# Kernel optimization log

Measured on AMD Instinct MI355X. Metric: run time of the kernel, lower is better.

The kernel has to match this reference:

```python
import jax, jax.numpy as jnp
import numpy as np

B, V = 256, 128000
NEG_INF = jnp.float32(-1e30)


def setup_inputs() -> dict:
    key = jax.random.key(0)
    k1, k2, k3 = jax.random.split(key, 3)
    logits = jax.random.normal(k1, (B, V), dtype=jnp.float32) * 2.0
    k = jax.random.randint(k2, (B,), 1, 65)                     # top-k in [1, 64]
    p = 0.5 + 0.5 * jax.random.uniform(k3, (B,), jnp.float32)   # top-p in [0.5, 1.0]
    return {"logits": logits, "k": k, "p": p}


def reference(logits, k, p):
    # softmax over vocab (rbln_top_k_top_p_sample: probs = softmax(logits))
    probs = jax.nn.softmax(logits, axis=-1)                      # [B, V]

    # sort probs descending (torch.ops.rbln.top_k_top_p semantics)
    order = jnp.argsort(-probs, axis=-1)                         # [B, V]
    sp = jnp.take_along_axis(probs, order, axis=-1)              # sorted probs, desc

    ranks = jnp.arange(V)
    topk_mask = ranks[None, :] < k[:, None]                      # keep top-k ranks

    csum = jnp.cumsum(sp, axis=-1)
    # keep tokens whose cumulative mass BEFORE them is < p (always keeps rank 0)
    topp_mask = (csum - sp) < p[:, None]

    keep = topk_mask & topp_mask                                 # [B, V] in sorted space
    filtered = jnp.where(keep, sp, 0.0)
    filtered = filtered / jnp.sum(filtered, axis=-1, keepdims=True)

    # sample from the renormalized filtered distribution (seed=42 as in module)
    logp = jnp.where(keep, jnp.log(jnp.maximum(filtered, 1e-38)), NEG_INF)
    sampled_rank = jax.random.categorical(jax.random.key(42), logp, axis=-1)  # [B]
    sampled = jnp.take_along_axis(order, sampled_rank[:, None], axis=-1)[:, 0]
    return sampled
```

## Files before the change

kernel.cpp:

```cpp
#include <hip/hip_runtime.h>
#include <stdint.h>

#define V 128000
#define V4 (V / 4)
#define BROWS 256
#define CAP 2048
#define NTHREADS 1024
#define T0 16.0f

__device__ __forceinline__ unsigned rotl32(unsigned x, int d) {
  return (x << d) | (x >> (32 - d));
}

__device__ __forceinline__ uint2 threefry2x32(unsigned x0, unsigned x1) {
  const unsigned k0 = 0u, k1 = 42u;
  const unsigned k2 = k0 ^ k1 ^ 0x1BD11BDAu;
  x0 += k0; x1 += k1;
#define TF_RND(r) { x0 += x1; x1 = rotl32(x1, r); x1 ^= x0; }
  TF_RND(13) TF_RND(15) TF_RND(26) TF_RND(6)
  x0 += k1; x1 += k2 + 1u;
  TF_RND(17) TF_RND(29) TF_RND(16) TF_RND(24)
  x0 += k2; x1 += k0 + 2u;
  TF_RND(13) TF_RND(15) TF_RND(26) TF_RND(6)
  x0 += k0; x1 += k1 + 3u;
  TF_RND(17) TF_RND(29) TF_RND(16) TF_RND(24)
  x0 += k1; x1 += k2 + 4u;
  TF_RND(13) TF_RND(15) TF_RND(26) TF_RND(6)
  x0 += k2; x1 += k0 + 5u;
#undef TF_RND
  return make_uint2(x0, x1);
}

__device__ __forceinline__ float gumbel_at(unsigned flat) {
  uint2 r = threefry2x32(0u, flat);
  unsigned bits = r.x ^ r.y;
  float f = __uint_as_float((bits >> 9) | 0x3F800000u) - 1.0f;
  const float TINY = 1.17549435e-38f;
  float u = fmaxf(TINY, f + TINY);
  return -logf(-logf(u));
}

__device__ __forceinline__ unsigned fkey(float v) {
  unsigned u = __float_as_uint(v);
  return (u & 0x80000000u) ? ~u : (u | 0x80000000u);
}
__device__ __forceinline__ float fkey_inv(unsigned u) {
  unsigned r = (u & 0x80000000u) ? (u & 0x7FFFFFFFu) : ~u;
  return __uint_as_float(r);
}

extern "C" __global__ void __launch_bounds__(NTHREADS)
topk_topp_sample_kernel(const float* __restrict__ logits,
                        const int* __restrict__ kin,
                        const float* __restrict__ pin,
                        int* __restrict__ out) {
  const int b = blockIdx.x;
  const int tid = threadIdx.x;

  __shared__ unsigned long long cand[CAP];
  __shared__ unsigned long long topkeys[64];
  __shared__ float zpart[NTHREADS / 64];
  __shared__ float sh_sp[64];
  __shared__ float sh_g[64];
  __shared__ int sh_idx[64];
  __shared__ int cnt;
  __shared__ float shZ;

  const float4* row4 = (const float4*)(logits + (size_t)b * V);
  float T = 6.0f;

  if (tid == 0) cnt = 0;
  __syncthreads();

  const float L2E = 1.44269504088896340736f;
  const float NB  = -16.0f * 1.44269504088896340736f;
  float zs0 = 0.0f, zs1 = 0.0f;

#define PROCV(vv, ii)                                                          \
  {                                                                            \
    float4 v = (vv);                                                           \
    zs0 += __builtin_amdgcn_exp2f(__builtin_fmaf(v.x, L2E, NB));               \
    zs1 += __builtin_amdgcn_exp2f(__builtin_fmaf(v.y, L2E, NB));               \
    zs0 += __builtin_amdgcn_exp2f(__builtin_fmaf(v.z, L2E, NB));               \
    zs1 += __builtin_amdgcn_exp2f(__builtin_fmaf(v.w, L2E, NB));               \
    int base = (ii) * 4;                                                       \
    if (v.x > T) { int pos = atomicAdd(&cnt, 1); if (pos < CAP) cand[pos] = ((unsigned long long)fkey(v.x) << 32) | (unsigned long long)(unsigned)(~(unsigned)(base + 0)); } \
    if (v.y > T) { int pos = atomicAdd(&cnt, 1); if (pos < CAP) cand[pos] = ((unsigned long long)fkey(v.y) << 32) | (unsigned long long)(unsigned)(~(unsigned)(base + 1)); } \
    if (v.z > T) { int pos = atomicAdd(&cnt, 1); if (pos < CAP) cand[pos] = ((unsigned long long)fkey(v.z) << 32) | (unsigned long long)(unsigned)(~(unsigned)(base + 2)); } \
    if (v.w > T) { int pos = atomicAdd(&cnt, 1); if (pos < CAP) cand[pos] = ((unsigned long long)fkey(v.w) << 32) | (unsigned long long)(unsigned)(~(unsigned)(base + 3)); } \
  }

  {
    int i = tid;
    for (; i + NTHREADS < V4; i += 2 * NTHREADS) {
      float4 a = row4[i];
      float4 c = row4[i + NTHREADS];
      PROCV(a, i);
      PROCV(c, i + NTHREADS);
    }
    if (i < V4) {
      float4 a = row4[i];
      PROCV(a, i);
    }
  }
  float s = zs0 + zs1;

#pragma unroll
  for (int off = 32; off > 0; off >>= 1) s += __shfl_down(s, off);
  if ((tid & 63) == 0) zpart[tid >> 6] = s;
  __syncthreads();
  if (tid == 0) {
    float z = 0.0f;
    for (int w = 0; w < NTHREADS / 64; ++w) z += zpart[w];
    shZ = z;
  }
  __syncthreads();

  int attempts = 0;
  while (true) {
    int n = cnt;
    if ((n >= 64 && n <= CAP) || attempts >= 24) break;
    T = (n < 64) ? (T - 2.0f) : (T + 1.0f);
    ++attempts;
    __syncthreads();
    if (tid == 0) cnt = 0;
    __syncthreads();
    for (int i = tid; i < V4; i += NTHREADS) {
      float4 v = row4[i];
      int base = i * 4;
      if (v.x > T) { int pos = atomicAdd(&cnt, 1); if (pos < CAP) cand[pos] = ((unsigned long long)fkey(v.x) << 32) | (unsigned long long)(unsigned)(~(unsigned)(base + 0)); }
      if (v.y > T) { int pos = atomicAdd(&cnt, 1); if (pos < CAP) cand[pos] = ((unsigned long long)fkey(v.y) << 32) | (unsigned long long)(unsigned)(~(unsigned)(base + 1)); }
      if (v.z > T) { int pos = atomicAdd(&cnt, 1); if (pos < CAP) cand[pos] = ((unsigned long long)fkey(v.z) << 32) | (unsigned long long)(unsigned)(~(unsigned)(base + 2)); }
      if (v.w > T) { int pos = atomicAdd(&cnt, 1); if (pos < CAP) cand[pos] = ((unsigned long long)fkey(v.w) << 32) | (unsigned long long)(unsigned)(~(unsigned)(base + 3)); }
    }
    __syncthreads();
  }

  int N = cnt < CAP ? cnt : CAP;

  for (int i = tid; i < N; i += NTHREADS) {
    unsigned long long ki = cand[i];
    int rank = 0;
    for (int j = 0; j < N; ++j) rank += (cand[j] > ki) ? 1 : 0;
    if (rank < 64) topkeys[rank] = ki;
  }
  __syncthreads();

  int M = N < 64 ? N : 64;

  if (tid < M) {
    unsigned long long key = topkeys[tid];
    float v = fkey_inv((unsigned)(key >> 32));
    sh_sp[tid] = expf(v - T0) / shZ;
    sh_idx[tid] = (int)(~((unsigned)(key & 0xFFFFFFFFull)));
    sh_g[tid] = gumbel_at((unsigned)((size_t)b * V + tid));
  }
  __syncthreads();

  if (tid == 0) {
    int kk = kin[b];
    float pp = pin[b];
    float c = 0.0f, S = 0.0f;
    unsigned long long keepmask = 0ull;
    for (int r = 0; r < M; ++r) {
      float sp = sh_sp[r];
      c += sp;
      if (r < kk && (c - sp) < pp) {
        S += sp;
        keepmask |= (1ull << r);
      }
    }
    float best = -1e38f;
    int besti = sh_idx[0];
    for (int r = 0; r < M; ++r) {
      if (!(keepmask & (1ull << r))) continue;
      float lp = logf(fmaxf(sh_sp[r] / S, 1e-38f));
      float y = lp + sh_g[r];
      if (y > best) { best = y; besti = sh_idx[r]; }
    }
    out[b] = besti;
  }
}

extern "C" void kernel_launch(void* const* d_in, const int* in_sizes, int n_in,
                              void* d_out, int out_size, void* d_ws, size_t ws_size,
                              hipStream_t stream) {
  const float* logits = (const float*)d_in[0];
  const int* k = (const int*)d_in[1];
  const float* p = (const float*)d_in[2];
  int* out = (int*)d_out;
  (void)in_sizes; (void)n_in; (void)out_size; (void)d_ws; (void)ws_size;
  topk_topp_sample_kernel<<<BROWS, NTHREADS, 0, stream>>>(logits, k, p, out);
}
```

Baseline: 202.7 us.

## Split row scan across eight segment blocks, then merge candidates per row

The single 1024-thread-block-per-row kernel becomes two kernels. The first launches eight 256-thread blocks per row, and each computes a partial softmax denominator and gathers logits above a threshold into a workspace. The second kernel merges those partial results per row, rank-sorts the candidates and samples, falling back to a full-row rescan if any segment overflows or too few candidates were found. The aim is more blocks in flight to saturate memory bandwidth, at the cost of a second launch and a workspace round-trip.

Measured after the change: 213.8 us. 5.5% more time.

```diff
diff --git a/kernel.cpp b/kernel.cpp
--- a/kernel.cpp
+++ b/kernel.cpp
@@ -2,11 +2,17 @@
 #include <stdint.h>
 
 #define V 128000
-#define V4 (V / 4)
 #define BROWS 256
-#define CAP 2048
-#define NTHREADS 1024
+#define SEGS 8
+#define SEGLEN (V / SEGS)
+#define SEG4 (SEGLEN / 4)
+#define CAPSEG 512
+#define CAPB 4096
+#define NT_A 256
+#define NT_B 256
 #define T0 16.0f
+
+typedef unsigned long long u64;
 
 __device__ __forceinline__ unsigned rotl32(unsigned x, int d) {
   return (x << d) | (x >> (32 - d));
@@ -49,29 +55,24 @@
   return __uint_as_float(r);
 }
 
-extern "C" __global__ void __launch_bounds__(NTHREADS)
-topk_topp_sample_kernel(const float* __restrict__ logits,
-                        const int* __restrict__ kin,
-                        const float* __restrict__ pin,
-                        int* __restrict__ out) {
-  const int b = blockIdx.x;
+extern "C" __global__ void __launch_bounds__(NT_A)
+scan_seg_kernel(const float* __restrict__ logits,
+                int* __restrict__ g_cnt, float* __restrict__ g_z,
+                u64* __restrict__ g_cand) {
+  const int bid = blockIdx.x;
+  const int row = bid >> 3, seg = bid & 7;
   const int tid = threadIdx.x;
 
-  __shared__ unsigned long long cand[CAP];
-  __shared__ unsigned long long topkeys[64];
-  __shared__ float zpart[NTHREADS / 64];
-  __shared__ float sh_sp[64];
-  __shared__ float sh_g[64];
-  __shared__ int sh_idx[64];
-  __shared__ int cnt;
-  __shared__ float shZ;
-
-  const float4* row4 = (const float4*)(logits + (size_t)b * V);
-  float T = 6.0f;
-
-  if (tid == 0) cnt = 0;
-  __syncthreads();
-
+  __shared__ u64 lcand[CAPSEG];
+  __shared__ int lcnt;
+  __shared__ float wz[NT_A / 64];
+
+  if (tid == 0) lcnt = 0;
+  __syncthreads();
+
+  const float4* p4 = (const float4*)(logits + (size_t)row * V) + seg * SEG4;
+  const int ebase = seg * SEGLEN;
+  const float T = 6.0f;
   const float L2E = 1.44269504088896340736f;
   const float NB  = -16.0f * 1.44269504088896340736f;
   float zs0 = 0.0f, zs1 = 0.0f;
@@ -83,63 +84,120 @@
     zs1 += __builtin_amdgcn_exp2f(__builtin_fmaf(v.y, L2E, NB));               \
     zs0 += __builtin_amdgcn_exp2f(__builtin_fmaf(v.z, L2E, NB));               \
     zs1 += __builtin_amdgcn_exp2f(__builtin_fmaf(v.w, L2E, NB));               \
-    int base = (ii) * 4;                                                       \
-    if (v.x > T) { int pos = atomicAdd(&cnt, 1); if (pos < CAP) cand[pos] = ((unsigned long long)fkey(v.x) << 32) | (unsigned long long)(unsigned)(~(unsigned)(base + 0)); } \
-    if (v.y > T) { int pos = atomicAdd(&cnt, 1); if (pos < CAP) cand[pos] = ((unsigned long long)fkey(v.y) << 32) | (unsigned long long)(unsigned)(~(unsigned)(base + 1)); } \
-    if (v.z > T) { int pos = atomicAdd(&cnt, 1); if (pos < CAP) cand[pos] = ((unsigned long long)fkey(v.z) << 32) | (unsigned long long)(unsigned)(~(unsigned)(base + 2)); } \
-    if (v.w > T) { int pos = atomicAdd(&cnt, 1); if (pos < CAP) cand[pos] = ((unsigned long long)fkey(v.w) << 32) | (unsigned long long)(unsigned)(~(unsigned)(base + 3)); } \
+    int eb = ebase + (ii) * 4;                                                 \
+    if (v.x > T) { int pos = atomicAdd(&lcnt, 1); if (pos < CAPSEG) lcand[pos] = ((u64)fkey(v.x) << 32) | (u64)(unsigned)(~(unsigned)(eb + 0)); } \
+    if (v.y > T) { int pos = atomicAdd(&lcnt, 1); if (pos < CAPSEG) lcand[pos] = ((u64)fkey(v.y) << 32) | (u64)(unsigned)(~(unsigned)(eb + 1)); } \
+    if (v.z > T) { int pos = atomicAdd(&lcnt, 1); if (pos < CAPSEG) lcand[pos] = ((u64)fkey(v.z) << 32) | (u64)(unsigned)(~(unsigned)(eb + 2)); } \
+    if (v.w > T) { int pos = atomicAdd(&lcnt, 1); if (pos < CAPSEG) lcand[pos] = ((u64)fkey(v.w) << 32) | (u64)(unsigned)(~(unsigned)(eb + 3)); } \
   }
 
   {
     int i = tid;
-    for (; i + NTHREADS < V4; i += 2 * NTHREADS) {
-      float4 a = row4[i];
-      float4 c = row4[i + NTHREADS];
+    for (; i + NT_A < SEG4; i += 2 * NT_A) {
+      float4 a = p4[i];
+      float4 c = p4[i + NT_A];
       PROCV(a, i);
-      PROCV(c, i + NTHREADS);
-    }
-    if (i < V4) {
-      float4 a = row4[i];
+      PROCV(c, i + NT_A);
+    }
+    if (i < SEG4) {
+      float4 a = p4[i];
       PROCV(a, i);
     }
   }
+#undef PROCV
+
   float s = zs0 + zs1;
-
 #pragma unroll
   for (int off = 32; off > 0; off >>= 1) s += __shfl_down(s, off);
-  if ((tid & 63) == 0) zpart[tid >> 6] = s;
-  __syncthreads();
+  if ((tid & 63) == 0) wz[tid >> 6] = s;
+  __syncthreads();
+
+  int n = lcnt;
+  int nc = n < CAPSEG ? n : CAPSEG;
+  u64* dst = g_cand + (size_t)bid * CAPSEG;
+  for (int i = tid; i < nc; i += NT_A) dst[i] = lcand[i];
   if (tid == 0) {
     float z = 0.0f;
-    for (int w = 0; w < NTHREADS / 64; ++w) z += zpart[w];
+    for (int w = 0; w < NT_A / 64; ++w) z += wz[w];
+    g_z[bid] = z;
+    g_cnt[bid] = n;
+  }
+}
+
+extern "C" __global__ void __launch_bounds__(NT_B)
+sample_row_kernel(const float* __restrict__ logits,
+                  const int* __restrict__ kin, const float* __restrict__ pin,
+                  int* __restrict__ out,
+                  const int* __restrict__ g_cnt, const float* __restrict__ g_z,
+                  const u64* __restrict__ g_cand) {
+  const int row = blockIdx.x;
+  const int tid = threadIdx.x;
+
+  __shared__ u64 cand[CAPB];
+  __shared__ u64 topkeys[64];
+  __shared__ float sh_sp[64];
+  __shared__ float sh_g[64];
+  __shared__ int sh_idx[64];
+  __shared__ int shCnt[SEGS], shOff[SEGS];
+  __shared__ float shZ;
+  __shared__ int shN, shSlow, scnt;
+
+  if (tid < SEGS) shCnt[tid] = g_cnt[row * SEGS + tid];
+  __syncthreads();
+  if (tid == 0) {
+    int off = 0, ovf = 0;
+    float z = 0.0f;
+    for (int s = 0; s < SEGS; ++s) {
+      shOff[s] = off;
+      int c = shCnt[s];
+      if (c > CAPSEG) ovf = 1;
+      off += (c < CAPSEG ? c : CAPSEG);
+      z += g_z[row * SEGS + s];
+    }
+    shN = off;
     shZ = z;
-  }
-  __syncthreads();
-
-  int attempts = 0;
-  while (true) {
-    int n = cnt;
-    if ((n >= 64 && n <= CAP) || attempts >= 24) break;
-    T = (n < 64) ? (T - 2.0f) : (T + 1.0f);
-    ++attempts;
-    __syncthreads();
-    if (tid == 0) cnt = 0;
-    __syncthreads();
-    for (int i = tid; i < V4; i += NTHREADS) {
-      float4 v = row4[i];
-      int base = i * 4;
-      if (v.x > T) { int pos = atomicAdd(&cnt, 1); if (pos < CAP) cand[pos] = ((unsigned long long)fkey(v.x) << 32) | (unsigned long long)(unsigned)(~(unsigned)(base + 0)); }
-      if (v.y > T) { int pos = atomicAdd(&cnt, 1); if (pos < CAP) cand[pos] = ((unsigned long long)fkey(v.y) << 32) | (unsigned long long)(unsigned)(~(unsigned)(base + 1)); }
-      if (v.z > T) { int pos = atomicAdd(&cnt, 1); if (pos < CAP) cand[pos] = ((unsigned long long)fkey(v.z) << 32) | (unsigned long long)(unsigned)(~(unsigned)(base + 2)); }
-      if (v.w > T) { int pos = atomicAdd(&cnt, 1); if (pos < CAP) cand[pos] = ((unsigned long long)fkey(v.w) << 32) | (unsigned long long)(unsigned)(~(unsigned)(base + 3)); }
-    }
-    __syncthreads();
-  }
-
-  int N = cnt < CAP ? cnt : CAP;
-
-  for (int i = tid; i < N; i += NTHREADS) {
-    unsigned long long ki = cand[i];
+    shSlow = (ovf || off < 64) ? 1 : 0;
+  }
+  __syncthreads();
+
+  int N;
+  if (!shSlow) {
+    for (int s = 0; s < SEGS; ++s) {
+      int c = shCnt[s];
+      c = c < CAPSEG ? c : CAPSEG;
+      const u64* src = g_cand + (size_t)(row * SEGS + s) * CAPSEG;
+      int off = shOff[s];
+      for (int i = tid; i < c; i += NT_B) cand[off + i] = src[i];
+    }
+    N = shN;
+  } else {
+    const float4* p4 = (const float4*)(logits + (size_t)row * V);
+    float T = 6.0f;
+    int attempts = 0;
+    while (true) {
+      if (tid == 0) scnt = 0;
+      __syncthreads();
+      for (int i = tid; i < V / 4; i += NT_B) {
+        float4 v = p4[i];
+        int eb = i * 4;
+        if (v.x > T) { int pos = atomicAdd(&scnt, 1); if (pos < CAPB) cand[pos] = ((u64)fkey(v.x) << 32) | (u64)(unsigned)(~(unsigned)(eb + 0)); }
+        if (v.y > T) { int pos = atomicAdd(&scnt, 1); if (pos < CAPB) cand[pos] = ((u64)fkey(v.y) << 32) | (u64)(unsigned)(~(unsigned)(eb + 1)); }
+        if (v.z > T) { int pos = atomicAdd(&scnt, 1); if (pos < CAPB) cand[pos] = ((u64)fkey(v.z) << 32) | (u64)(unsigned)(~(unsigned)(eb + 2)); }
+        if (v.w > T) { int pos = atomicAdd(&scnt, 1); if (pos < CAPB) cand[pos] = ((u64)fkey(v.w) << 32) | (u64)(unsigned)(~(unsigned)(eb + 3)); }
+      }
+      __syncthreads();
+      int n = scnt;
+      if ((n >= 64 && n <= CAPB) || attempts >= 24) break;
+      T = (n < 64) ? (T - 2.0f) : (T + 1.0f);
+      ++attempts;
+      __syncthreads();
+    }
+    N = scnt < CAPB ? scnt : CAPB;
+  }
+  __syncthreads();
+
+  for (int i = tid; i < N; i += NT_B) {
+    u64 ki = cand[i];
     int rank = 0;
     for (int j = 0; j < N; ++j) rank += (cand[j] > ki) ? 1 : 0;
     if (rank < 64) topkeys[rank] = ki;
@@ -149,19 +207,19 @@
   int M = N < 64 ? N : 64;
 
   if (tid < M) {
-    unsigned long long key = topkeys[tid];
+    u64 key = topkeys[tid];
     float v = fkey_inv((unsigned)(key >> 32));
     sh_sp[tid] = expf(v - T0) / shZ;
     sh_idx[tid] = (int)(~((unsigned)(key & 0xFFFFFFFFull)));
-    sh_g[tid] = gumbel_at((unsigned)((size_t)b * V + tid));
+    sh_g[tid] = gumbel_at((unsigned)((size_t)row * V + tid));
   }
   __syncthreads();
 
   if (tid == 0) {
-    int kk = kin[b];
-    float pp = pin[b];
+    int kk = kin[row];
+    float pp = pin[row];
     float c = 0.0f, S = 0.0f;
-    unsigned long long keepmask = 0ull;
+    u64 keepmask = 0ull;
     for (int r = 0; r < M; ++r) {
       float sp = sh_sp[r];
       c += sp;
@@ -178,7 +236,7 @@
       float y = lp + sh_g[r];
       if (y > best) { best = y; besti = sh_idx[r]; }
     }
-    out[b] = besti;
+    out[row] = besti;
   }
 }
 
@@ -189,6 +247,13 @@
   const int* k = (const int*)d_in[1];
   const float* p = (const float*)d_in[2];
   int* out = (int*)d_out;
-  (void)in_sizes; (void)n_in; (void)out_size; (void)d_ws; (void)ws_size;
-  topk_topp_sample_kernel<<<BROWS, NTHREADS, 0, stream>>>(logits, k, p, out);
-}
+  (void)in_sizes; (void)n_in; (void)out_size; (void)ws_size;
+
+  char* ws = (char*)d_ws;
+  int* g_cnt = (int*)ws;
+  float* g_z = (float*)(ws + 16384);
+  u64* g_cand = (u64*)(ws + 32768);
+
+  scan_seg_kernel<<<BROWS * SEGS, NT_A, 0, stream>>>(logits, g_cnt, g_z, g_cand);
+  sample_row_kernel<<<BROWS, NT_B, 0, stream>>>(logits, k, p, out, g_cnt, g_z, g_cand);
+}
```
